# Optimization experiments

Measured on AMD Instinct MI355X. Metric: run time of the kernel, lower is better.

Reference implementation:

```python
import jax, jax.numpy as jnp
import numpy as np

N_NODES = 100000
N_EDGES = 1600000
IN_DIM = 64
OUT_DIM = 64
BN_EPS = 1e-5


def batchnorm(h, gamma, beta):
    # BatchNorm1d in training mode: per-feature batch stats, biased variance
    mean = jnp.mean(h, axis=0)
    var = jnp.mean((h - mean) ** 2, axis=0)
    return gamma * (h - mean) * jax.lax.rsqrt(var + BN_EPS) + beta


def setup_inputs() -> dict:
    key = jax.random.key(0)
    ks = jax.random.split(key, 4)
    x = jax.random.normal(ks[0], (N_NODES, IN_DIM), dtype=jnp.float32)
    edge_index = jax.random.randint(ks[1], (2, N_EDGES), 0, N_NODES, dtype=jnp.int32)
    epsilon = jnp.asarray(0.1, dtype=jnp.float32)
    # Linear weights stored [in, out] (transpose of torch layout)
    W1 = jax.random.normal(ks[2], (IN_DIM, 2 * OUT_DIM), dtype=jnp.float32) * (1.0 / np.sqrt(IN_DIM))
    b1 = jnp.zeros((2 * OUT_DIM,), dtype=jnp.float32)
    g1 = jnp.ones((2 * OUT_DIM,), dtype=jnp.float32)
    be1 = jnp.zeros((2 * OUT_DIM,), dtype=jnp.float32)
    W2 = jax.random.normal(ks[3], (2 * OUT_DIM, OUT_DIM), dtype=jnp.float32) * (1.0 / np.sqrt(2 * OUT_DIM))
    b2 = jnp.zeros((OUT_DIM,), dtype=jnp.float32)
    g2 = jnp.ones((OUT_DIM,), dtype=jnp.float32)
    be2 = jnp.zeros((OUT_DIM,), dtype=jnp.float32)
    return {"x": x, "edge_index": edge_index, "epsilon": epsilon,
            "W1": W1, "b1": b1, "g1": g1, "be1": be1,
            "W2": W2, "b2": b2, "g2": g2, "be2": be2}


def reference(x, edge_index, epsilon, W1, b1, g1, be1, W2, b2, g2, be2):
    src, dst = edge_index[0], edge_index[1]
    # gather messages from src, scatter-add into dst  [N, D]
    neighbor_sum = jnp.zeros_like(x).at[dst].add(x[src])
    combined = (1.0 + epsilon) * x + neighbor_sum
    h = combined @ W1 + b1            # [N, 2*out_dim]
    h = jax.nn.relu(batchnorm(h, g1, be1))
    h = h @ W2 + b2                   # [N, out_dim]
    return batchnorm(h, g2, be2)
```

## Files before the change

kernel.cpp:

```cpp
#include <hip/hip_runtime.h>

#define N_NODES 100000
#define N_EDGES 1600000
#define IN_DIM 64
#define H_DIM 128
#define OUT_DIM 64
#define BN_EPS 1e-5f
#define CAP 64
#define BIN_SHIFT 9
#define BIN_NODES 512
#define NB 256
#define NBIN_BLOCKS ((N_NODES + BIN_NODES - 1) / BIN_NODES)

#define OFF_XB     0
#define OFF_BINNED 3200000
#define OFF_H1     6400000
#define OFF_H2     12800000
#define OFF_STATS  19200000
#define S1SUM 0
#define S1SQ  128
#define S2SUM 256
#define S2SQ  320

#define DEV_ATOMIC_ADD(p, v) __hip_atomic_fetch_add((p), (v), __ATOMIC_RELAXED, __HIP_MEMORY_SCOPE_AGENT)

typedef __attribute__((ext_vector_type(8))) short short8;
typedef __attribute__((ext_vector_type(4))) float f32x4;

__device__ __forceinline__ unsigned short f2bf(float f) {
  union { float f; unsigned u; } v; v.f = f;
  unsigned r = v.u + 0x7FFFu + ((v.u >> 16) & 1u);
  return (unsigned short)(r >> 16);
}
__device__ __forceinline__ float bflo(unsigned v) { union { unsigned u; float f; } t; t.u = v << 16; return t.f; }
__device__ __forceinline__ float bfhi(unsigned v) { union { unsigned u; float f; } t; t.u = v & 0xFFFF0000u; return t.f; }

__device__ __forceinline__ void acc8(float* a, uint4 v) {
  a[0] += bflo(v.x); a[1] += bfhi(v.x); a[2] += bflo(v.y); a[3] += bfhi(v.y);
  a[4] += bflo(v.z); a[5] += bfhi(v.z); a[6] += bflo(v.w); a[7] += bfhi(v.w);
}
__device__ __forceinline__ uint4 pack8(const float* a) {
  uint4 o;
  o.x = (unsigned)f2bf(a[0]) | ((unsigned)f2bf(a[1]) << 16);
  o.y = (unsigned)f2bf(a[2]) | ((unsigned)f2bf(a[3]) << 16);
  o.z = (unsigned)f2bf(a[4]) | ((unsigned)f2bf(a[5]) << 16);
  o.w = (unsigned)f2bf(a[6]) | ((unsigned)f2bf(a[7]) << 16);
  return o;
}

__global__ __launch_bounds__(256) void k_prep(const float* __restrict__ x,
                                              unsigned short* __restrict__ xb,
                                              const int* __restrict__ ei,
                                              int* __restrict__ bhist) {
  __shared__ int h[NB];
  const int tid = threadIdx.x;
  h[tid] = 0;
  #pragma unroll
  for (int j = 0; j < 8; ++j) {
    int i = blockIdx.x * 2048 + j * 256 + tid;
    if (i < N_NODES * IN_DIM / 4) {
      float4 v = ((const float4*)x)[i];
      ushort4 o;
      o.x = f2bf(v.x); o.y = f2bf(v.y); o.z = f2bf(v.z); o.w = f2bf(v.w);
      *(ushort4*)(xb + i * 4) = o;
    }
  }
  __syncthreads();
  #pragma unroll
  for (int j = 0; j < 8; ++j) {
    int e = blockIdx.x * 2048 + j * 256 + tid;
    if (e < N_EDGES) atomicAdd(&h[ei[N_EDGES + e] >> BIN_SHIFT], 1);
  }
  __syncthreads();
  if (h[tid]) DEV_ATOMIC_ADD(&bhist[tid], h[tid]);
}

__global__ __launch_bounds__(256) void k_scan256(const int* __restrict__ bhist,
                                                 int* __restrict__ boff,
                                                 int* __restrict__ bcur) {
  __shared__ int s[NB];
  const int tid = threadIdx.x;
  int v = bhist[tid];
  s[tid] = v;
  __syncthreads();
  for (int d = 1; d < NB; d <<= 1) {
    int t = (tid >= d) ? s[tid - d] : 0;
    __syncthreads();
    s[tid] += t;
    __syncthreads();
  }
  int incl = s[tid];
  boff[tid] = incl - v;
  if (tid == NB - 1) boff[NB] = incl;
  bcur[tid] = incl - v;
}

__global__ __launch_bounds__(256) void k_bsplit(const int* __restrict__ ei,
                                                int* __restrict__ bcur,
                                                int2* __restrict__ binned) {
  __shared__ int lcnt[NB];
  __shared__ int lofs[NB];
  __shared__ int lbase[NB];
  __shared__ int sc[NB];
  __shared__ int2 staged[2048];
  const int tid = threadIdx.x;
  lcnt[tid] = 0;
  __syncthreads();
  int src[8], dst[8], rk[8];
  #pragma unroll
  for (int j = 0; j < 8; ++j) {
    int e = blockIdx.x * 2048 + j * 256 + tid;
    if (e < N_EDGES) {
      src[j] = ei[e];
      dst[j] = ei[N_EDGES + e];
      rk[j] = atomicAdd(&lcnt[dst[j] >> BIN_SHIFT], 1);
    } else {
      src[j] = -1;
    }
  }
  __syncthreads();
  int v = lcnt[tid];
  sc[tid] = v;
  __syncthreads();
  for (int d = 1; d < NB; d <<= 1) {
    int t = (tid >= d) ? sc[tid - d] : 0;
    __syncthreads();
    sc[tid] += t;
    __syncthreads();
  }
  lofs[tid] = sc[tid] - v;
  if (v > 0) lbase[tid] = DEV_ATOMIC_ADD(&bcur[tid], v);
  __syncthreads();
  #pragma unroll
  for (int j = 0; j < 8; ++j) {
    if (src[j] >= 0) {
      int b = dst[j] >> BIN_SHIFT;
      staged[lofs[b] + rk[j]] = make_int2(src[j], dst[j]);
    }
  }
  int nv = sc[NB - 1];
  __syncthreads();
  for (int i = tid; i < nv; i += 256) {
    int2 e = staged[i];
    int b = e.y >> BIN_SHIFT;
    binned[lbase[b] + (i - lofs[b])] = e;
  }
}

__global__ __launch_bounds__(512) void k_bfill(const int* __restrict__ boff,
                                               const int2* __restrict__ binned,
                                               int* __restrict__ cnt,
                                               int* __restrict__ srcl) {
  __shared__ int lcnt[BIN_NODES];
  const int tid = threadIdx.x;
  for (int i = tid; i < BIN_NODES; i += 512) lcnt[i] = 0;
  __syncthreads();
  const int b = blockIdx.x;
  const int s = boff[b], e = boff[b + 1];
  const int base = b * BIN_NODES;
  for (int i = s + tid; i < e; i += 512) {
    int2 ed = binned[i];
    int pos = atomicAdd(&lcnt[ed.y - base], 1);
    if (pos < CAP) srcl[ed.y * CAP + pos] = ed.x;
  }
  __syncthreads();
  for (int i = tid; i < BIN_NODES; i += 512) {
    int node = base + i;
    if (node < N_NODES) cnt[node] = lcnt[i];
  }
}

#define APAD 72
__global__ __launch_bounds__(256) void k_fuse1(const unsigned short* __restrict__ xb,
                                               const float* __restrict__ eps,
                                               const int* __restrict__ cnt,
                                               const int* __restrict__ srcl,
                                               const float* __restrict__ W1,
                                               const float* __restrict__ b1,
                                               unsigned short* __restrict__ h1,
                                               float* __restrict__ stats) {
  __shared__ unsigned short As[128 * APAD];
  __shared__ unsigned short Ws[128 * APAD];
  __shared__ float red[4][128];
  const int tid = threadIdx.x;
  const int wv = tid >> 6, lane = tid & 63;
  const int quad = lane >> 4, ln = lane & 15;
  const int rowBase = blockIdx.x * 128;

  #pragma unroll
  for (int it = 0; it < 8; ++it) {
    int idx = it * 256 + tid;
    int k = idx >> 5, n4 = idx & 31;
    float4 wv1 = *(const float4*)(W1 + k * 128 + n4 * 4);
    Ws[(n4 * 4 + 0) * APAD + k] = f2bf(wv1.x);
    Ws[(n4 * 4 + 1) * APAD + k] = f2bf(wv1.y);
    Ws[(n4 * 4 + 2) * APAD + k] = f2bf(wv1.z);
    Ws[(n4 * 4 + 3) * APAD + k] = f2bf(wv1.w);
  }

  {
    int row = tid >> 1;
    int half = tid & 1;
    int node = rowBase + row;
    float a[32];
    #pragma unroll
    for (int i = 0; i < 32; ++i) a[i] = 0.f;
    if (node < N_NODES) {
      const unsigned short* bp = xb + node * 64 + half * 32;
      acc8(a, *(const uint4*)bp);
      acc8(a + 8, *(const uint4*)(bp + 8));
      acc8(a + 16, *(const uint4*)(bp + 16));
      acc8(a + 24, *(const uint4*)(bp + 24));
      float e = 1.0f + eps[0];
      #pragma unroll
      for (int i = 0; i < 32; ++i) a[i] *= e;
      int deg = cnt[node];
      if (deg > CAP) deg = CAP;
      const int* sl = srcl + node * CAP;
      int j = 0;
      for (; j + 2 <= deg; j += 2) {
        const unsigned short* p0 = xb + sl[j] * 64 + half * 32;
        const unsigned short* p1 = xb + sl[j + 1] * 64 + half * 32;
        uint4 v0 = *(const uint4*)p0;
        uint4 v1 = *(const uint4*)(p0 + 8);
        uint4 v2 = *(const uint4*)(p0 + 16);
        uint4 v3 = *(const uint4*)(p0 + 24);
        uint4 w0 = *(const uint4*)p1;
        uint4 w1 = *(const uint4*)(p1 + 8);
        uint4 w2 = *(const uint4*)(p1 + 16);
        uint4 w3 = *(const uint4*)(p1 + 24);
        acc8(a, v0); acc8(a + 8, v1); acc8(a + 16, v2); acc8(a + 24, v3);
        acc8(a, w0); acc8(a + 8, w1); acc8(a + 16, w2); acc8(a + 24, w3);
      }
      if (j < deg) {
        const unsigned short* p0 = xb + sl[j] * 64 + half * 32;
        acc8(a, *(const uint4*)p0);
        acc8(a + 8, *(const uint4*)(p0 + 8));
        acc8(a + 16, *(const uint4*)(p0 + 16));
        acc8(a + 24, *(const uint4*)(p0 + 24));
      }
    }
    unsigned short* ap = &As[row * APAD + half * 32];
    *(uint4*)ap = pack8(a);
    *(uint4*)(ap + 8) = pack8(a + 8);
    *(uint4*)(ap + 16) = pack8(a + 16);
    *(uint4*)(ap + 24) = pack8(a + 24);
  }
  __syncthreads();

  f32x4 acc[2][8];
  #pragma unroll
  for (int mt = 0; mt < 2; ++mt) {
    #pragma unroll
    for (int nt = 0; nt < 8; ++nt) acc[mt][nt] = (f32x4)0.0f;
  }
  const int rw = wv * 32;
  #pragma unroll
  for (int kb = 0; kb < 2; ++kb) {
    short8 a0 = *(short8*)&As[(rw + ln) * APAD + kb * 32 + quad * 8];
    short8 a1 = *(short8*)&As[(rw + 16 + ln) * APAD + kb * 32 + quad * 8];
    #pragma unroll
    for (int nt = 0; nt < 8; ++nt) {
      short8 b = *(short8*)&Ws[(nt * 16 + ln) * APAD + kb * 32 + quad * 8];
      acc[0][nt] = __builtin_amdgcn_mfma_f32_16x16x32_bf16(a0, b, acc[0][nt], 0, 0, 0);
      acc[1][nt] = __builtin_amdgcn_mfma_f32_16x16x32_bf16(a1, b, acc[1][nt], 0, 0, 0);
    }
  }

  float bias[8], s[8], q[8];
  #pragma unroll
  for (int nt = 0; nt < 8; ++nt) { bias[nt] = b1[nt * 16 + ln]; s[nt] = 0.f; q[nt] = 0.f; }
  #pragma unroll
  for (int mt = 0; mt < 2; ++mt) {
    #pragma unroll
    for (int i = 0; i < 4; ++i) {
      int gRow = rowBase + rw + mt * 16 + quad * 4 + i;
      if (gRow < N_NODES) {
        #pragma unroll
        for (int nt = 0; nt < 8; ++nt) {
          float v = acc[mt][nt][i] + bias[nt];
          h1[gRow * 128 + nt * 16 + ln] = f2bf(v);
          s[nt] += v; q[nt] += v * v;
        }
      }
    }
  }
  #pragma unroll
  for (int nt = 0; nt < 8; ++nt) {
    s[nt] += __shfl_xor(s[nt], 16); s[nt] += __shfl_xor(s[nt], 32);
    q[nt] += __shfl_xor(q[nt], 16); q[nt] += __shfl_xor(q[nt], 32);
  }
  if (lane < 16) {
    #pragma unroll
    for (int nt = 0; nt < 8; ++nt) red[wv][nt * 16 + ln] = s[nt];
  }
  __syncthreads();
  if (tid < 128) DEV_ATOMIC_ADD(&stats[S1SUM + tid],
                                red[0][tid] + red[1][tid] + red[2][tid] + red[3][tid]);
  __syncthreads();
  if (lane < 16) {
    #pragma unroll
    for (int nt = 0; nt < 8; ++nt) red[wv][nt * 16 + ln] = q[nt];
  }
  __syncthreads();
  if (tid < 128) DEV_ATOMIC_ADD(&stats[S1SQ + tid],
                                red[0][tid] + red[1][tid] + red[2][tid] + red[3][tid]);
}

#define WPAD 136
__global__ __launch_bounds__(256) void k_gemm2(const unsigned short* __restrict__ h1,
                                               const float* __restrict__ W2,
                                               const float* __restrict__ b2,
                                               const float* __restrict__ g1,
                                               const float* __restrict__ be1,
                                               unsigned short* __restrict__ h2,
                                               float* __restrict__ stats) {
  __shared__ unsigned short As[128 * APAD];
  __shared__ unsigned short Ws[64 * WPAD];
  __shared__ float red[4][64];
  __shared__ float scL[128], shL[128];
  const int tid = threadIdx.x;
  const int wv = tid >> 6, lane = tid & 63;
  const int quad = lane >> 4, ln = lane & 15;
  const int rowBase = blockIdx.x * 128;

  if (tid < 128) {
    float mean = stats[S1SUM + tid] * (1.0f / N_NODES);
    float var = stats[S1SQ + tid] * (1.0f / N_NODES) - mean * mean;
    var = fmaxf(var, 0.0f);
    float sc = g1[tid] * rsqrtf(var + BN_EPS);
    scL[tid] = sc;
    shL[tid] = be1[tid] - mean * sc;
  }
  #pragma unroll
  for (int it = 0; it < 8; ++it) {
    int idx = it * 256 + tid;
    int k = idx >> 4, n4 = idx & 15;
    float4 wv2 = *(const float4*)(W2 + k * 64 + n4 * 4);
    Ws[(n4 * 4 + 0) * WPAD + k] = f2bf(wv2.x);
    Ws[(n4 * 4 + 1) * WPAD + k] = f2bf(wv2.y);
    Ws[(n4 * 4 + 2) * WPAD + k] = f2bf(wv2.z);
    Ws[(n4 * 4 + 3) * WPAD + k] = f2bf(wv2.w);
  }

  f32x4 acc[2][4];
  #pragma unroll
  for (int mt = 0; mt < 2; ++mt) {
    #pragma unroll
    for (int nt = 0; nt < 4; ++nt) acc[mt][nt] = (f32x4)0.0f;
  }
  const int rw = wv * 32;

  for (int kc = 0; kc < 2; ++kc) {
    __syncthreads();
    #pragma unroll
    for (int it = 0; it < 4; ++it) {
      int idx = it * 256 + tid;
      int row = idx >> 3, ch = idx & 7;
      int gRow = rowBase + row;
      uint4 u = (gRow < N_NODES) ? *(const uint4*)(h1 + gRow * 128 + kc * 64 + ch * 8)
                                 : make_uint4(0, 0, 0, 0);
      int kb = kc * 64 + ch * 8;
      float f0 = fmaxf(bflo(u.x) * scL[kb + 0] + shL[kb + 0], 0.f);
      float f1 = fmaxf(bfhi(u.x) * scL[kb + 1] + shL[kb + 1], 0.f);
      float f2 = fmaxf(bflo(u.y) * scL[kb + 2] + shL[kb + 2], 0.f);
      float f3 = fmaxf(bfhi(u.y) * scL[kb + 3] + shL[kb + 3], 0.f);
      float f4 = fmaxf(bflo(u.z) * scL[kb + 4] + shL[kb + 4], 0.f);
      float f5 = fmaxf(bfhi(u.z) * scL[kb + 5] + shL[kb + 5], 0.f);
      float f6 = fmaxf(bflo(u.w) * scL[kb + 6] + shL[kb + 6], 0.f);
      float f7 = fmaxf(bfhi(u.w) * scL[kb + 7] + shL[kb + 7], 0.f);
      uint4 o;
      o.x = (unsigned)f2bf(f0) | ((unsigned)f2bf(f1) << 16);
      o.y = (unsigned)f2bf(f2) | ((unsigned)f2bf(f3) << 16);
      o.z = (unsigned)f2bf(f4) | ((unsigned)f2bf(f5) << 16);
      o.w = (unsigned)f2bf(f6) | ((unsigned)f2bf(f7) << 16);
      *(uint4*)&As[row * APAD + ch * 8] = o;
    }
    __syncthreads();
    #pragma unroll
    for (int kb = 0; kb < 2; ++kb) {
      short8 a0 = *(short8*)&As[(rw + ln) * APAD + kb * 32 + quad * 8];
      short8 a1 = *(short8*)&As[(rw + 16 + ln) * APAD + kb * 32 + quad * 8];
      #pragma unroll
      for (int nt = 0; nt < 4; ++nt) {
        short8 b = *(short8*)&Ws[(nt * 16 + ln) * WPAD + kc * 64 + kb * 32 + quad * 8];
        acc[0][nt] = __builtin_amdgcn_mfma_f32_16x16x32_bf16(a0, b, acc[0][nt], 0, 0, 0);
        acc[1][nt] = __builtin_amdgcn_mfma_f32_16x16x32_bf16(a1, b, acc[1][nt], 0, 0, 0);
      }
    }
  }

  float bias[4], s[4], q[4];
  #pragma unroll
  for (int nt = 0; nt < 4; ++nt) { bias[nt] = b2[nt * 16 + ln]; s[nt] = 0.f; q[nt] = 0.f; }
  #pragma unroll
  for (int mt = 0; mt < 2; ++mt) {
    #pragma unroll
    for (int i = 0; i < 4; ++i) {
      int gRow = rowBase + rw + mt * 16 + quad * 4 + i;
      if (gRow < N_NODES) {
        #pragma unroll
        for (int nt = 0; nt < 4; ++nt) {
          float v = acc[mt][nt][i] + bias[nt];
          h2[gRow * 64 + nt * 16 + ln] = f2bf(v);
          s[nt] += v; q[nt] += v * v;
        }
      }
    }
  }
  #pragma unroll
  for (int nt = 0; nt < 4; ++nt) {
    s[nt] += __shfl_xor(s[nt], 16); s[nt] += __shfl_xor(s[nt], 32);
    q[nt] += __shfl_xor(q[nt], 16); q[nt] += __shfl_xor(q[nt], 32);
  }
  if (lane < 16) {
    #pragma unroll
    for (int nt = 0; nt < 4; ++nt) red[wv][nt * 16 + ln] = s[nt];
  }
  __syncthreads();
  if (tid < 64) DEV_ATOMIC_ADD(&stats[S2SUM + tid],
                               red[0][tid] + red[1][tid] + red[2][tid] + red[3][tid]);
  __syncthreads();
  if (lane < 16) {
    #pragma unroll
    for (int nt = 0; nt < 4; ++nt) red[wv][nt * 16 + ln] = q[nt];
  }
  __syncthreads();
  if (tid < 64) DEV_ATOMIC_ADD(&stats[S2SQ + tid],
                               red[0][tid] + red[1][tid] + red[2][tid] + red[3][tid]);
}

__global__ __launch_bounds__(256) void k_out(const unsigned short* __restrict__ h2,
                                             const float* __restrict__ stats,
                                             const float* __restrict__ g2,
                                             const float* __restrict__ be2,
                                             float* __restrict__ out) {
  __shared__ float scL[64], shL[64];
  const int tid = threadIdx.x;
  if (tid < 64) {
    float mean = stats[S2SUM + tid] * (1.0f / N_NODES);
    float var = stats[S2SQ + tid] * (1.0f / N_NODES) - mean * mean;
    var = fmaxf(var, 0.0f);
    float sc = g2[tid] * rsqrtf(var + BN_EPS);
    scL[tid] = sc;
    shL[tid] = be2[tid] - mean * sc;
  }
  __syncthreads();
  int i = blockIdx.x * 256 + tid;
  if (i < N_NODES * OUT_DIM / 4) {
    int c = i & 15;
    uint2 u = *(const uint2*)(h2 + i * 4);
    float4 v = {bflo(u.x), bfhi(u.x), bflo(u.y), bfhi(u.y)};
    float4 sc = ((const float4*)scL)[c];
    float4 sh = ((const float4*)shL)[c];
    v.x = v.x * sc.x + sh.x;
    v.y = v.y * sc.y + sh.y;
    v.z = v.z * sc.z + sh.z;
    v.w = v.w * sc.w + sh.w;
    ((float4*)out)[i] = v;
  }
}

extern "C" void kernel_launch(void* const* d_in, const int* in_sizes, int n_in,
                              void* d_out, int out_size, void* d_ws, size_t ws_size,
                              hipStream_t stream) {
  const float* x   = (const float*)d_in[0];
  const int*   ei  = (const int*)d_in[1];
  const float* eps = (const float*)d_in[2];
  const float* W1  = (const float*)d_in[3];
  const float* b1  = (const float*)d_in[4];
  const float* g1  = (const float*)d_in[5];
  const float* be1 = (const float*)d_in[6];
  const float* W2  = (const float*)d_in[7];
  const float* b2  = (const float*)d_in[8];
  const float* g2  = (const float*)d_in[9];
  const float* be2 = (const float*)d_in[10];

  float* ws = (float*)d_ws;
  unsigned short* xb     = (unsigned short*)(ws + OFF_XB);
  int2*           binned = (int2*)(ws + OFF_BINNED);
  unsigned short* h1     = (unsigned short*)(ws + OFF_H1);
  int*            srcl   = (int*)(ws + OFF_H1);
  unsigned short* h2     = (unsigned short*)(ws + OFF_H2);
  int*            cnt    = (int*)(ws + OFF_H2);
  float*          stats  = ws + OFF_STATS;
  int*            bhist  = (int*)(stats + 768);
  int*            boff   = (int*)(stats + 1024);
  int*            bcur   = (int*)(stats + 1288);
  float*          out    = (float*)d_out;

  hipMemsetAsync(stats, 0, 1024 * sizeof(float), stream);

  const int edgeGrid = (N_EDGES + 2047) / 2048;
  const int gemmGrid = (N_NODES + 127) / 128;
  k_prep<<<edgeGrid, 256, 0, stream>>>(x, xb, ei, bhist);
  k_scan256<<<1, NB, 0, stream>>>(bhist, boff, bcur);
  k_bsplit<<<edgeGrid, 256, 0, stream>>>(ei, bcur, binned);
  k_bfill<<<NBIN_BLOCKS, 512, 0, stream>>>(boff, binned, cnt, srcl);
  k_fuse1<<<gemmGrid, 256, 0, stream>>>(xb, eps, cnt, srcl, W1, b1, h1, stats);
  k_gemm2<<<gemmGrid, 256, 0, stream>>>(h1, W2, b2, g1, be1, h2, stats);
  k_out<<<(N_NODES * OUT_DIM / 4 + 255) / 256, 256, 0, stream>>>(h2, stats, g2, be2, out);
}
```

Baseline: 254.2 us.

## Pretranspose weights to bf16 once and halve GEMM row tiles to 64

The fp32-to-bf16 conversion and transpose of W1 and W2 move into the prep kernel, which writes them once to workspace. Both GEMM kernels now read B fragments straight from global memory (L2-resident) instead of building a per-block LDS copy. Row tiles shrink from 128 to 64 nodes, and the gather uses four threads per node with 16 features each. This doubles the block count and cuts LDS and register use per block, aiming at better occupancy and latency hiding for the gather. The cost is more blocks issuing stats atomics and uncached global weight fragment loads on every MFMA step.

```diff
diff --git a/kernel.cpp b/kernel.cpp
--- a/kernel.cpp
+++ b/kernel.cpp
@@ -16,6 +16,8 @@
 #define OFF_BINNED 3200000
 #define OFF_H1     6400000
 #define OFF_H2     12800000
+#define OFF_W1T    16000000
+#define OFF_W2T    16004096
 #define OFF_STATS  19200000
 #define S1SUM 0
 #define S1SQ  128
@@ -51,7 +53,11 @@
 __global__ __launch_bounds__(256) void k_prep(const float* __restrict__ x,
                                               unsigned short* __restrict__ xb,
                                               const int* __restrict__ ei,
-                                              int* __restrict__ bhist) {
+                                              int* __restrict__ bhist,
+                                              const float* __restrict__ W1,
+                                              const float* __restrict__ W2,
+                                              unsigned short* __restrict__ W1t,
+                                              unsigned short* __restrict__ W2t) {
   __shared__ int h[NB];
   const int tid = threadIdx.x;
   h[tid] = 0;
@@ -63,6 +69,20 @@
       ushort4 o;
       o.x = f2bf(v.x); o.y = f2bf(v.y); o.z = f2bf(v.z); o.w = f2bf(v.w);
       *(ushort4*)(xb + i * 4) = o;
+    }
+  }
+  if (blockIdx.x < 16) {
+    #pragma unroll
+    for (int t = 0; t < 4; ++t) {
+      int gid = blockIdx.x * 1024 + t * 256 + tid;
+      if (gid < 8192) {
+        int n = gid >> 6, k = gid & 63;
+        W1t[n * 64 + k] = f2bf(W1[k * 128 + n]);
+      } else {
+        int g = gid - 8192;
+        int n = g >> 7, k = g & 127;
+        W2t[n * 128 + k] = f2bf(W2[k * 64 + n]);
+      }
     }
   }
   __syncthreads();
@@ -175,95 +195,68 @@
                                                const float* __restrict__ eps,
                                                const int* __restrict__ cnt,
                                                const int* __restrict__ srcl,
-                                               const float* __restrict__ W1,
+                                               const unsigned short* __restrict__ W1t,
                                                const float* __restrict__ b1,
                                                unsigned short* __restrict__ h1,
                                                float* __restrict__ stats) {
-  __shared__ unsigned short As[128 * APAD];
-  __shared__ unsigned short Ws[128 * APAD];
+  __shared__ unsigned short As[64 * APAD];
   __shared__ float red[4][128];
   const int tid = threadIdx.x;
   const int wv = tid >> 6, lane = tid & 63;
   const int quad = lane >> 4, ln = lane & 15;
-  const int rowBase = blockIdx.x * 128;
-
-  #pragma unroll
-  for (int it = 0; it < 8; ++it) {
-    int idx = it * 256 + tid;
-    int k = idx >> 5, n4 = idx & 31;
-    float4 wv1 = *(const float4*)(W1 + k * 128 + n4 * 4);
-    Ws[(n4 * 4 + 0) * APAD + k] = f2bf(wv1.x);
-    Ws[(n4 * 4 + 1) * APAD + k] = f2bf(wv1.y);
-    Ws[(n4 * 4 + 2) * APAD + k] = f2bf(wv1.z);
-    Ws[(n4 * 4 + 3) * APAD + k] = f2bf(wv1.w);
-  }
+  const int rowBase = blockIdx.x * 64;
 
   {
-    int row = tid >> 1;
-    int half = tid & 1;
-    int node = rowBase + row;
-    float a[32];
-    #pragma unroll
-    for (int i = 0; i < 32; ++i) a[i] = 0.f;
+    int r = tid >> 2;
+    int q = tid & 3;
+    int node = rowBase + r;
+    float a[16];
+    #pragma unroll
+    for (int i = 0; i < 16; ++i) a[i] = 0.f;
     if (node < N_NODES) {
-      const unsigned short* bp = xb + node * 64 + half * 32;
+      const unsigned short* bp = xb + node * 64 + q * 16;
       acc8(a, *(const uint4*)bp);
       acc8(a + 8, *(const uint4*)(bp + 8));
-      acc8(a + 16, *(const uint4*)(bp + 16));
-      acc8(a + 24, *(const uint4*)(bp + 24));
       float e = 1.0f + eps[0];
       #pragma unroll
-      for (int i = 0; i < 32; ++i) a[i] *= e;
+      for (int i = 0; i < 16; ++i) a[i] *= e;
       int deg = cnt[node];
       if (deg > CAP) deg = CAP;
       const int* sl = srcl + node * CAP;
       int j = 0;
       for (; j + 2 <= deg; j += 2) {
-        const unsigned short* p0 = xb + sl[j] * 64 + half * 32;
-        const unsigned short* p1 = xb + sl[j + 1] * 64 + half * 32;
+        const unsigned short* p0 = xb + sl[j] * 64 + q * 16;
+        const unsigned short* p1 = xb + sl[j + 1] * 64 + q * 16;
         uint4 v0 = *(const uint4*)p0;
         uint4 v1 = *(const uint4*)(p0 + 8);
-        uint4 v2 = *(const uint4*)(p0 + 16);
-        uint4 v3 = *(const uint4*)(p0 + 24);
         uint4 w0 = *(const uint4*)p1;
         uint4 w1 = *(const uint4*)(p1 + 8);
-        uint4 w2 = *(const uint4*)(p1 + 16);
-        uint4 w3 = *(const uint4*)(p1 + 24);
-        acc8(a, v0); acc8(a + 8, v1); acc8(a + 16, v2); acc8(a + 24, v3);
-        acc8(a, w0); acc8(a + 8, w1); acc8(a + 16, w2); acc8(a + 24, w3);
+        acc8(a, v0); acc8(a + 8, v1);
+        acc8(a, w0); acc8(a + 8, w1);
       }
       if (j < deg) {
-        const unsigned short* p0 = xb + sl[j] * 64 + half * 32;
+        const unsigned short* p0 = xb + sl[j] * 64 + q * 16;
         acc8(a, *(const uint4*)p0);
         acc8(a + 8, *(const uint4*)(p0 + 8));
-        acc8(a + 16, *(const uint4*)(p0 + 16));
-        acc8(a + 24, *(const uint4*)(p0 + 24));
-      }
-    }
-    unsigned short* ap = &As[row * APAD + half * 32];
+      }
+    }
+    unsigned short* ap = &As[r * APAD + q * 16];
     *(uint4*)ap = pack8(a);
     *(uint4*)(ap + 8) = pack8(a + 8);
-    *(uint4*)(ap + 16) = pack8(a + 16);
-    *(uint4*)(ap + 24) = pack8(a + 24);
-  }
-  __syncthreads();
-
-  f32x4 acc[2][8];
-  #pragma unroll
-  for (int mt = 0; mt < 2; ++mt) {
-    #pragma unroll
-    for (int nt = 0; nt < 8; ++nt) acc[mt][nt] = (f32x4)0.0f;
-  }
-  const int rw = wv * 32;
+  }
+  __syncthreads();
+
+  f32x4 acc[8];
+  #pragma unroll
+  for (int nt = 0; nt < 8; ++nt) acc[nt] = (f32x4)0.0f;
+  const int rw = wv * 16;
   #pragma unroll
   for (int kb = 0; kb < 2; ++kb) {
     short8 a0 = *(short8*)&As[(rw + ln) * APAD + kb * 32 + quad * 8];
-    short8 a1 = *(short8*)&As[(rw + 16 + ln) * APAD + kb * 32 + quad * 8];
     #pragma unroll
     for (int nt = 0; nt < 8; ++nt) {
-      short8 b = *(short8*)&Ws[(nt * 16 + ln) * APAD + kb * 32 + quad * 8];
-      acc[0][nt] = __builtin_amdgcn_mfma_f32_16x16x32_bf16(a0, b, acc[0][nt], 0, 0, 0);
-      acc[1][nt] = __builtin_amdgcn_mfma_f32_16x16x32_bf16(a1, b, acc[1][nt], 0, 0, 0);
+      short8 b = *(const short8*)(W1t + (nt * 16 + ln) * 64 + kb * 32 + quad * 8);
+      acc[nt] = __builtin_amdgcn_mfma_f32_16x16x32_bf16(a0, b, acc[nt], 0, 0, 0);
     }
   }
 
@@ -271,17 +264,14 @@
   #pragma unroll
   for (int nt = 0; nt < 8; ++nt) { bias[nt] = b1[nt * 16 + ln]; s[nt] = 0.f; q[nt] = 0.f; }
   #pragma unroll
-  for (int mt = 0; mt < 2; ++mt) {
-    #pragma unroll
-    for (int i = 0; i < 4; ++i) {
-      int gRow = rowBase + rw + mt * 16 + quad * 4 + i;
-      if (gRow < N_NODES) {
-        #pragma unroll
-        for (int nt = 0; nt < 8; ++nt) {
-          float v = acc[mt][nt][i] + bias[nt];
-          h1[gRow * 128 + nt * 16 + ln] = f2bf(v);
-          s[nt] += v; q[nt] += v * v;
-        }
+  for (int i = 0; i < 4; ++i) {
+    int gRow = rowBase + rw + quad * 4 + i;
+    if (gRow < N_NODES) {
+      #pragma unroll
+      for (int nt = 0; nt < 8; ++nt) {
+        float v = acc[nt][i] + bias[nt];
+        h1[gRow * 128 + nt * 16 + ln] = f2bf(v);
+        s[nt] += v; q[nt] += v * v;
       }
     }
   }
@@ -307,22 +297,20 @@
                                 red[0][tid] + red[1][tid] + red[2][tid] + red[3][tid]);
 }
 
-#define WPAD 136
 __global__ __launch_bounds__(256) void k_gemm2(const unsigned short* __restrict__ h1,
-                                               const float* __restrict__ W2,
+                                               const unsigned short* __restrict__ W2t,
                                                const float* __restrict__ b2,
                                                const float* __restrict__ g1,
                                                const float* __restrict__ be1,
                                                unsigned short* __restrict__ h2,
                                                float* __restrict__ stats) {
-  __shared__ unsigned short As[128 * APAD];
-  __shared__ unsigned short Ws[64 * WPAD];
+  __shared__ unsigned short As[64 * APAD];
   __shared__ float red[4][64];
   __shared__ float scL[128], shL[128];
   const int tid = threadIdx.x;
   const int wv = tid >> 6, lane = tid & 63;
   const int quad = lane >> 4, ln = lane & 15;
-  const int rowBase = blockIdx.x * 128;
+  const int rowBase = blockIdx.x * 64;
 
   if (tid < 128) {
     float mean = stats[S1SUM + tid] * (1.0f / N_NODES);
@@ -332,29 +320,16 @@
     scL[tid] = sc;
     shL[tid] = be1[tid] - mean * sc;
   }
-  #pragma unroll
-  for (int it = 0; it < 8; ++it) {
-    int idx = it * 256 + tid;
-    int k = idx >> 4, n4 = idx & 15;
-    float4 wv2 = *(const float4*)(W2 + k * 64 + n4 * 4);
-    Ws[(n4 * 4 + 0) * WPAD + k] = f2bf(wv2.x);
-    Ws[(n4 * 4 + 1) * WPAD + k] = f2bf(wv2.y);
-    Ws[(n4 * 4 + 2) * WPAD + k] = f2bf(wv2.z);
-    Ws[(n4 * 4 + 3) * WPAD + k] = f2bf(wv2.w);
-  }
-
-  f32x4 acc[2][4];
-  #pragma unroll
-  for (int mt = 0; mt < 2; ++mt) {
-    #pragma unroll
-    for (int nt = 0; nt < 4; ++nt) acc[mt][nt] = (f32x4)0.0f;
-  }
-  const int rw = wv * 32;
+
+  f32x4 acc[4];
+  #pragma unroll
+  for (int nt = 0; nt < 4; ++nt) acc[nt] = (f32x4)0.0f;
+  const int rw = wv * 16;
 
   for (int kc = 0; kc < 2; ++kc) {
     __syncthreads();
     #pragma unroll
-    for (int it = 0; it < 4; ++it) {
+    for (int it = 0; it < 2; ++it) {
       int idx = it * 256 + tid;
       int row = idx >> 3, ch = idx & 7;
       int gRow = rowBase + row;
@@ -380,12 +355,10 @@
     #pragma unroll
     for (int kb = 0; kb < 2; ++kb) {
       short8 a0 = *(short8*)&As[(rw + ln) * APAD + kb * 32 + quad * 8];
-      short8 a1 = *(short8*)&As[(rw + 16 + ln) * APAD + kb * 32 + quad * 8];
       #pragma unroll
       for (int nt = 0; nt < 4; ++nt) {
-        short8 b = *(short8*)&Ws[(nt * 16 + ln) * WPAD + kc * 64 + kb * 32 + quad * 8];
-        acc[0][nt] = __builtin_amdgcn_mfma_f32_16x16x32_bf16(a0, b, acc[0][nt], 0, 0, 0);
-        acc[1][nt] = __builtin_amdgcn_mfma_f32_16x16x32_bf16(a1, b, acc[1][nt], 0, 0, 0);
+        short8 b = *(const short8*)(W2t + (nt * 16 + ln) * 128 + kc * 64 + kb * 32 + quad * 8);
+        acc[nt] = __builtin_amdgcn_mfma_f32_16x16x32_bf16(a0, b, acc[nt], 0, 0, 0);
       }
     }
   }
@@ -394,17 +367,14 @@
   #pragma unroll
   for (int nt = 0; nt < 4; ++nt) { bias[nt] = b2[nt * 16 + ln]; s[nt] = 0.f; q[nt] = 0.f; }
   #pragma unroll
-  for (int mt = 0; mt < 2; ++mt) {
-    #pragma unroll
-    for (int i = 0; i < 4; ++i) {
-      int gRow = rowBase + rw + mt * 16 + quad * 4 + i;
-      if (gRow < N_NODES) {
-        #pragma unroll
-        for (int nt = 0; nt < 4; ++nt) {
-          float v = acc[mt][nt][i] + bias[nt];
-          h2[gRow * 64 + nt * 16 + ln] = f2bf(v);
-          s[nt] += v; q[nt] += v * v;
-        }
+  for (int i = 0; i < 4; ++i) {
+    int gRow = rowBase + rw + quad * 4 + i;
+    if (gRow < N_NODES) {
+      #pragma unroll
+      for (int nt = 0; nt < 4; ++nt) {
+        float v = acc[nt][i] + bias[nt];
+        h2[gRow * 64 + nt * 16 + ln] = f2bf(v);
+        s[nt] += v; q[nt] += v * v;
       }
     }
   }
@@ -483,6 +453,8 @@
   int*            srcl   = (int*)(ws + OFF_H1);
   unsigned short* h2     = (unsigned short*)(ws + OFF_H2);
   int*            cnt    = (int*)(ws + OFF_H2);
+  unsigned short* W1t    = (unsigned short*)(ws + OFF_W1T);
+  unsigned short* W2t    = (unsigned short*)(ws + OFF_W2T);
   float*          stats  = ws + OFF_STATS;
   int*            bhist  = (int*)(stats + 768);
   int*            boff   = (int*)(stats + 1024);
@@ -492,12 +464,12 @@
   hipMemsetAsync(stats, 0, 1024 * sizeof(float), stream);
 
   const int edgeGrid = (N_EDGES + 2047) / 2048;
-  const int gemmGrid = (N_NODES + 127) / 128;
-  k_prep<<<edgeGrid, 256, 0, stream>>>(x, xb, ei, bhist);
+  const int tileGrid = (N_NODES + 63) / 64;
+  k_prep<<<edgeGrid, 256, 0, stream>>>(x, xb, ei, bhist, W1, W2, W1t, W2t);
   k_scan256<<<1, NB, 0, stream>>>(bhist, boff, bcur);
   k_bsplit<<<edgeGrid, 256, 0, stream>>>(ei, bcur, binned);
   k_bfill<<<NBIN_BLOCKS, 512, 0, stream>>>(boff, binned, cnt, srcl);
-  k_fuse1<<<gemmGrid, 256, 0, stream>>>(xb, eps, cnt, srcl, W1, b1, h1, stats);
-  k_gemm2<<<gemmGrid, 256, 0, stream>>>(h1, W2, b2, g1, be1, h2, stats);
+  k_fuse1<<<tileGrid, 256, 0, stream>>>(xb, eps, cnt, srcl, W1t, b1, h1, stats);
+  k_gemm2<<<tileGrid, 256, 0, stream>>>(h1, W2t, b2, g1, be1, h2, stats);
   k_out<<<(N_NODES * OUT_DIM / 4 + 255) / 256, 256, 0, stream>>>(h2, stats, g2, be2, out);
 }
```

New measurement: 294.4 us. 1.16x slower.
